# Optimization experiments

Measured on AMD Instinct MI355X. Metric: run time of the kernel, lower is better.

The kernel has to match this reference:

```python
import jax, jax.numpy as jnp
import numpy as np

DIM = 256
HEADS = 8
CAMS = 6
MINSIZE = 25  # AdaptiveAvgPool2d output size = min(feature_map_size)


def layernorm(x, g, b, eps=1e-5):
    mu = x.mean(-1, keepdims=True)
    var = ((x - mu) ** 2).mean(-1, keepdims=True)
    return (x - mu) / jnp.sqrt(var + eps) * g + b


def setup_inputs() -> dict:
    key = jax.random.key(0)
    ks = jax.random.split(key, 16)
    d, n = DIM, CAMS
    s = 0.02
    inp = {}
    inp["q"] = jax.random.normal(ks[0], (2, n, d, 50, 50), jnp.float32)
    inp["k"] = jax.random.normal(ks[1], (2, n, d, 50, 50), jnp.float32)
    inp["v"] = jax.random.normal(ks[2], (2, n, d, 50, 50), jnp.float32)
    inp["Wq"] = jax.random.normal(ks[3], (d, d), jnp.float32) * s
    inp["bq"] = jnp.zeros((d,), jnp.float32)
    inp["Wk"] = jax.random.normal(ks[4], (d, d), jnp.float32) * s
    inp["bk"] = jnp.zeros((d,), jnp.float32)
    inp["Wv"] = jax.random.normal(ks[5], (d, d), jnp.float32) * s
    inp["bv"] = jnp.zeros((d,), jnp.float32)
    inp["Wproj"] = jax.random.normal(ks[6], (n * d, d), jnp.float32) * s
    inp["bproj"] = jnp.zeros((d,), jnp.float32)
    inp["Waddq"] = jax.random.normal(ks[7], (n * d, d), jnp.float32) * s
    inp["baddq"] = jnp.zeros((d,), jnp.float32)
    inp["W1"] = jax.random.normal(ks[8], (d, 2 * d), jnp.float32) * s
    inp["b1"] = jnp.zeros((2 * d,), jnp.float32)
    inp["W2"] = jax.random.normal(ks[9], (2 * d, d), jnp.float32) * s
    inp["b2"] = jnp.zeros((d,), jnp.float32)
    inp["g_pre"] = jnp.ones((n * d,), jnp.float32)
    inp["b_pre"] = jnp.zeros((n * d,), jnp.float32)
    inp["g_norm"] = jnp.ones((d,), jnp.float32)
    inp["b_norm"] = jnp.zeros((d,), jnp.float32)
    return inp


def reference(q, k, v, Wq, bq, Wk, bk, Wv, bv, Wproj, bproj, Waddq, baddq,
              W1, b1, W2, b2, g_pre, b_pre, g_norm, b_norm):
    B, n, d, H, W = q.shape
    m = HEADS
    dh = d // m
    Q = H * W

    # residual query path: (b n d H W) -> (b HW (n d)) -> add_qproj -> (b HW d)
    add_q = jnp.transpose(q, (0, 3, 4, 1, 2)).reshape(B, Q, n * d) @ Waddq + baddq

    # queries: (b n d H W) -> (b n HW d) -> to_q
    qf = jnp.transpose(q, (0, 1, 3, 4, 2)).reshape(B, n, Q, d) @ Wq + bq

    # adaptive avg pool to MINSIZE (exact 2x2 bins since 50 = 2*25)
    def pool(t):
        _, _, _, h, w = t.shape
        return t.reshape(B, n, d, MINSIZE, h // MINSIZE, MINSIZE, w // MINSIZE).mean((4, 6))

    kp = pool(k)  # (b n d 25 25)
    vp = pool(v)
    K = MINSIZE * MINSIZE
    # (avg pool commutes with the pointwise linear to_k/to_v)
    kf = jnp.transpose(kp, (0, 1, 3, 4, 2)).reshape(B, n, K, d) @ Wk + bk
    vf = jnp.transpose(vp, (0, 1, 3, 4, 2)).reshape(B, n, K, d) @ Wv + bv

    # split heads
    qh = qf.reshape(B, n, Q, m, dh)
    kh = kf.reshape(B, n, K, m, dh)
    vh = vf.reshape(B, n, K, m, dh)

    # per-camera scores, softmax jointly over concatenated camera keys
    scores = (dh ** -0.5) * jnp.einsum('bnqmd,bnkmd->bmqnk', qh, kh)  # (B,m,Q,n,K)
    attn = jax.nn.softmax(scores.reshape(B, m, Q, n * K), axis=-1).reshape(B, m, Q, n, K)

    # per-camera attention output, concat cams (and heads within each cam) -> (B,Q,n*d)
    out = jnp.einsum('bmqnk,bnkmd->bqnmd', attn, vh).reshape(B, Q, n * d)

    x = layernorm(out, g_pre, b_pre) @ Wproj + bproj  # (B,Q,d)
    x = x + add_q
    h1 = jax.nn.gelu(x @ W1 + b1, approximate=False)
    x = x + layernorm(h1 @ W2 + b2, g_norm, b_norm)
    return jnp.transpose(x.reshape(B, H, W, d), (0, 3, 1, 2))  # (B,d,H,W)
```

## Files before the change

### kernel.cpp

```cpp
#include <hip/hip_runtime.h>
#include <math.h>

#define BATCH 2
#define NCAM 6
#define DIM 256
#define HEADS 8
#define DH 32
#define HW 2500
#define KP 625
#define NDIM (NCAM*DIM)

#define SCALE_LOG2E 0.25503488494404f

typedef __attribute__((ext_vector_type(8))) short short8;
typedef __attribute__((ext_vector_type(4))) float f32x4;

__device__ __forceinline__ short f2bf(float f) {
    union { float f; unsigned u; } v; v.f = f;
    unsigned r = v.u + 0x7fffu + ((v.u >> 16) & 1u);
    return (short)(r >> 16);
}
__device__ __forceinline__ float bf2f(short h) {
    union { unsigned u; float f; } v; v.u = ((unsigned)(unsigned short)h) << 16;
    return v.f;
}
__device__ __forceinline__ float exp2_hw(float x) {
    return __builtin_amdgcn_exp2f(x);
}

struct WJ { const float* src; short* dst; int K, N; };
struct WArgs { WJ j[7]; };

__global__ __launch_bounds__(256) void prep_all(
    const float* __restrict__ q, const float* __restrict__ k,
    const float* __restrict__ v, short* __restrict__ qbf,
    short* __restrict__ kpbf, short* __restrict__ vpbf, WArgs wa)
{
    __shared__ float t[32][33];
    const int tx = threadIdx.x & 31, ty = threadIdx.x >> 5;
    int i = blockIdx.x;
    if (i < 7584) {
        int slab = i / 632, rem = i % 632;
        int hwB = (rem % 79) * 32, dB = (rem / 79) * 32;
        const float* src = q + (size_t)slab * 640000;
#pragma unroll
        for (int ii = 0; ii < 32; ii += 8) {
            int hw = hwB + tx;
            t[ty + ii][tx] = (hw < HW) ? src[(size_t)(dB + ty + ii) * HW + hw] : 0.f;
        }
        __syncthreads();
#pragma unroll
        for (int ii = 0; ii < 32; ii += 8) {
            int hw = hwB + ty + ii;
            if (hw < HW)
                qbf[((size_t)slab * HW + hw) * DIM + dB + tx] = f2bf(t[tx][ty + ii]);
        }
    } else if (i < 11424) {
        int i2 = i - 7584;
        const float* base; short* dst;
        if (i2 < 1920) { base = k; dst = kpbf; }
        else           { base = v; dst = vpbf; i2 -= 1920; }
        int slab = i2 / 160, rem = i2 % 160;
        int kpB = (rem % 20) * 32, dB = (rem / 20) * 32;
        const float* src = base + (size_t)slab * 640000;
        dst += (size_t)slab * (KP * DIM);
#pragma unroll
        for (int ii = 0; ii < 32; ii += 8) {
            int kp = kpB + tx;
            float val = 0.f;
            if (kp < KP) {
                int r2 = (kp / 25) * 2, c2 = (kp % 25) * 2;
                const float* p0 = src + (size_t)(dB + ty + ii) * HW + r2 * 50 + c2;
                val = 0.25f * (p0[0] + p0[1] + p0[50] + p0[51]);
            }
            t[ty + ii][tx] = val;
        }
        __syncthreads();
#pragma unroll
        for (int ii = 0; ii < 32; ii += 8) {
            int kp = kpB + ty + ii;
            if (kp < KP)
                dst[(size_t)kp * DIM + dB + tx] = f2bf(t[tx][ty + ii]);
        }
    } else {
        int wi = i - 11424;
        WJ jb = wa.j[0];
        for (int jj = 0; jj < 7; jj++) {
            jb = wa.j[jj];
            int cnt = (jb.K >> 5) * (jb.N >> 5);
            if (wi < cnt) break;
            wi -= cnt;
        }
        int tn = jb.N >> 5;
        int nB = (wi % tn) * 32, kB = (wi / tn) * 32;
#pragma unroll
        for (int ii = 0; ii < 32; ii += 8)
            t[ty + ii][tx] = jb.src[(size_t)(kB + ty + ii) * jb.N + nB + tx];
        __syncthreads();
#pragma unroll
        for (int ii = 0; ii < 32; ii += 8)
            jb.dst[(size_t)(nB + ty + ii) * jb.K + kB + tx] = f2bf(t[tx][ty + ii]);
    }
}

struct GJob { const short* A; const short* Bt; const float* bias;
              short* Cb; float* Cf; int M, Ks, Kl, kOff, mode; float smul; };
struct GArgs { GJob j[5]; int base[6]; };

__global__ __launch_bounds__(256) void gemm_in(GArgs ga) {
    int bid;
    {
        const int nwg = ga.base[5];
        int orig = blockIdx.x;
        int q8 = nwg >> 3, r8 = nwg & 7;
        int xcd = orig & 7, idx = orig >> 3;
        bid = (xcd < r8 ? xcd * (q8 + 1) : r8 * (q8 + 1) + (xcd - r8) * q8) + idx;
    }
    int jj = 0;
    while (bid >= ga.base[jj + 1]) jj++;
    GJob jb = ga.j[jj];
    const int local = bid - ga.base[jj];

    __shared__ short As[128 * 32];
    __shared__ short Bs[64 * 32];

    const int tid  = threadIdx.x;
    const int nB   = (local & 3) * 64;
    const int rB   = (local >> 2) * 128;
    const int w    = tid >> 6;
    const int lane = tid & 63;
    const int l15  = lane & 15;
    const int quad = lane >> 4;
    const int M = jb.M, Ks = jb.Ks, Kl = jb.Kl, kOff = jb.kOff;

    f32x4 acc[2][4];
#pragma unroll
    for (int i = 0; i < 2; i++)
#pragma unroll
        for (int jt = 0; jt < 4; jt++) acc[i][jt] = (f32x4){0.f, 0.f, 0.f, 0.f};

    const int ra = tid >> 1, k0 = (tid & 1) * 16;
    const int rga = rB + ra;
    const int bb = rga / 2500, hwp = rga % 2500;
    const int nb_ = tid >> 2, gkb = tid & 3;

    short8 pa0 = {0,0,0,0,0,0,0,0}, pa1 = pa0, pb = pa0;
    if (rga < M) {
        if (jb.mode) {
            int kk = kOff + k0;
            int cam = kk >> 8, c = kk & 255;
            const short* p = &jb.A[(((size_t)(bb * 6 + cam)) * HW + hwp) * DIM + c];
            pa0 = *(const short8*)p; pa1 = *(const short8*)(p + 8);
        } else {
            const short* p = &jb.A[(size_t)rga * Ks + kOff + k0];
            pa0 = *(const short8*)p; pa1 = *(const short8*)(p + 8);
        }
    }
    pb = *(const short8*)&jb.Bt[(size_t)(nB + nb_) * Ks + kOff + gkb * 8];

    for (int kB = 0; kB < Kl; kB += 32) {
        __syncthreads();
        {
            int g0 = k0 >> 3;
            *(short8*)&As[ra * 32 + ((g0 ^ (ra & 3)) << 3)]       = pa0;
            *(short8*)&As[ra * 32 + (((g0 + 1) ^ (ra & 3)) << 3)] = pa1;
            *(short8*)&Bs[nb_ * 32 + ((gkb ^ (nb_ & 3)) << 3)]    = pb;
        }
        __syncthreads();
        int kN = kB + 32;
        if (kN < Kl) {
            if (rga < M) {
                if (jb.mode) {
                    int kk = kOff + kN + k0;
                    int cam = kk >> 8, c = kk & 255;
                    const short* p = &jb.A[(((size_t)(bb * 6 + cam)) * HW + hwp) * DIM + c];
                    pa0 = *(const short8*)p; pa1 = *(const short8*)(p + 8);
                } else {
                    const short* p = &jb.A[(size_t)rga * Ks + kOff + kN + k0];
                    pa0 = *(const short8*)p; pa1 = *(const short8*)(p + 8);
                }
            }
            pb = *(const short8*)&jb.Bt[(size_t)(nB + nb_) * Ks + kOff + kN + gkb * 8];
        }
        short8 af[2], bfr[4];
#pragma unroll
        for (int i = 0; i < 2; i++) {
            int m = w * 32 + i * 16 + l15;
            af[i] = *(const short8*)&As[m * 32 + ((quad ^ (m & 3)) << 3)];
        }
#pragma unroll
        for (int jt = 0; jt < 4; jt++) {
            int n = jt * 16 + l15;
            bfr[jt] = *(const short8*)&Bs[n * 32 + ((quad ^ (n & 3)) << 3)];
        }
#pragma unroll
        for (int i = 0; i < 2; i++)
#pragma unroll
            for (int jt = 0; jt < 4; jt++)
                acc[i][jt] = __builtin_amdgcn_mfma_f32_16x16x32_bf16(
                    af[i], bfr[jt], acc[i][jt], 0, 0, 0);
    }
#pragma unroll
    for (int i = 0; i < 2; i++) {
        int rbase = rB + w * 32 + i * 16 + quad * 4;
#pragma unroll
        for (int jt = 0; jt < 4; jt++) {
            int col = nB + jt * 16 + l15;
            float bcol = jb.bias ? jb.bias[col] : 0.f;
#pragma unroll
            for (int reg = 0; reg < 4; reg++) {
                int rr = rbase + reg;
                if (rr < M) {
                    float vv = (acc[i][jt][reg] + bcol) * jb.smul;
                    if (jb.Cb) jb.Cb[(size_t)rr * 256 + col] = f2bf(vv);
                    else       jb.Cf[(size_t)rr * 256 + col] = vv;
                }
            }
        }
    }
}

template<int EPI, int WF32, int WBF>
__global__ __launch_bounds__(256) void mgemm_bf(
    const short* __restrict__ A, const short* __restrict__ Bt,
    const float* __restrict__ bias, const float* __restrict__ res,
    const float* __restrict__ res2,
    float* __restrict__ C, short* __restrict__ C2, int M, int N, int K)
{
    __shared__ short As[128 * 32];
    __shared__ short Bs[64 * 32];

    const int tid  = threadIdx.x;
    const int nB   = blockIdx.x * 64;
    const int rB   = blockIdx.y * 128;
    const int w    = tid >> 6;
    const int lane = tid & 63;
    const int l15  = lane & 15;
    const int quad = lane >> 4;

    f32x4 acc[2][4];
#pragma unroll
    for (int i = 0; i < 2; i++)
#pragma unroll
        for (int jt = 0; jt < 4; jt++) acc[i][jt] = (f32x4){0.f, 0.f, 0.f, 0.f};

    const int ra = tid >> 1, k0 = (tid & 1) * 16;
    const int rga = rB + ra;
    const int nb_ = tid >> 2, gkb = tid & 3;

    short8 pa0 = {0,0,0,0,0,0,0,0}, pa1 = pa0, pb = pa0;
    if (rga < M) {
        const short* p = &A[(size_t)rga * K + k0];
        pa0 = *(const short8*)p; pa1 = *(const short8*)(p + 8);
    }
    pb = *(const short8*)&Bt[(size_t)(nB + nb_) * K + gkb * 8];

    for (int kB = 0; kB < K; kB += 32) {
        __syncthreads();
        {
            int g0 = k0 >> 3;
            *(short8*)&As[ra * 32 + ((g0 ^ (ra & 3)) << 3)]       = pa0;
            *(short8*)&As[ra * 32 + (((g0 + 1) ^ (ra & 3)) << 3)] = pa1;
            *(short8*)&Bs[nb_ * 32 + ((gkb ^ (nb_ & 3)) << 3)]    = pb;
        }
        __syncthreads();
        int kN = kB + 32;
        if (kN < K) {
            if (rga < M) {
                const short* p = &A[(size_t)rga * K + kN + k0];
                pa0 = *(const short8*)p; pa1 = *(const short8*)(p + 8);
            }
            pb = *(const short8*)&Bt[(size_t)(nB + nb_) * K + kN + gkb * 8];
        }
        short8 af[2], bfr[4];
#pragma unroll
        for (int i = 0; i < 2; i++) {
            int m = w * 32 + i * 16 + l15;
            af[i] = *(const short8*)&As[m * 32 + ((quad ^ (m & 3)) << 3)];
        }
#pragma unroll
        for (int jt = 0; jt < 4; jt++) {
            int n = jt * 16 + l15;
            bfr[jt] = *(const short8*)&Bs[n * 32 + ((quad ^ (n & 3)) << 3)];
        }
#pragma unroll
        for (int i = 0; i < 2; i++)
#pragma unroll
            for (int jt = 0; jt < 4; jt++)
                acc[i][jt] = __builtin_amdgcn_mfma_f32_16x16x32_bf16(
                    af[i], bfr[jt], acc[i][jt], 0, 0, 0);
    }
#pragma unroll
    for (int i = 0; i < 2; i++) {
        int rbase = rB + w * 32 + i * 16 + quad * 4;
#pragma unroll
        for (int jt = 0; jt < 4; jt++) {
            int col = nB + jt * 16 + l15;
            float bcol = bias[col];
#pragma unroll
            for (int reg = 0; reg < 4; reg++) {
                int rr = rbase + reg;
                if (rr < M) {
                    float vv = acc[i][jt][reg] + bcol;
                    if (EPI == 1) vv = 0.5f * vv * (1.f + erff(vv * 0.70710678118654752f));
                    if (EPI == 2) {
                        vv += res[(size_t)rr * N + col];
                        if (res2) vv += res2[(size_t)rr * N + col];
                    }
                    if (WF32) C[(size_t)rr * N + col] = vv;
                    if (WBF)  C2[(size_t)rr * N + col] = f2bf(vv);
                }
            }
        }
    }
}

#define TQA 64
#define CH 64
#define VSTR 72

__global__ __launch_bounds__(256) void attn_mfma(
    const short* __restrict__ qf, const short* __restrict__ kf,
    const short* __restrict__ vf, short* __restrict__ attn_out,
    float* __restrict__ Zp)
{
    const int qt  = blockIdx.x;
    const int bm  = blockIdx.y;
    const int cam = blockIdx.z;
    const int b = bm >> 3, m = bm & 7;
    const int q0 = qt * TQA;
    const int tid = threadIdx.x;
    const int w = tid >> 6, lane = tid & 63;
    const int l15 = lane & 15, quad = lane >> 4;

    __shared__ __align__(16) short Ks[CH][DH];
    __shared__ __align__(16) short Vt[DH][VSTR];

    const size_t slab = (size_t)(b * 6 + cam);

    int qrow = q0 + w * 16 + l15;
    int qcl  = qrow < HW ? qrow : HW - 1;
    const short8 aq = *(const short8*)&qf[(slab * HW + qcl) * DIM + m * DH + quad * 8];

    const short* kb = kf + slab * KP * DIM + m * DH;
    const short* vb = vf + slab * KP * DIM + m * DH;

    f32x4 oacc[2];
    oacc[0] = (f32x4){0.f, 0.f, 0.f, 0.f};
    oacc[1] = (f32x4){0.f, 0.f, 0.f, 0.f};
    float zp = 0.f;

    const int kl = tid >> 2, d8 = (tid & 3) * 8;
    const int jtw  = ((kl >> 5) & 1) | (((kl >> 2) & 1) << 1);
    const int rw   = (((kl >> 3) & 3) << 2) | (kl & 3);
    const int krow = jtw * 16 + rw;
    const int kp2 = tid >> 3, dv = (tid & 7) * 4;
    const int vcol2 = (((kp2 >> 2) ^ (dv >> 3)) << 3) | ((2 * kp2) & 7);

    for (int c0 = 0; c0 < KP; c0 += CH) {
        __syncthreads();
        {
            int key = c0 + kl;
            short8 kv8 = {0, 0, 0, 0, 0, 0, 0, 0};
            if (key < KP) kv8 = *(const short8*)&kb[(size_t)key * DIM + d8];
            *(short8*)&Ks[krow][d8] = kv8;

            int k0v = c0 + 2 * kp2;
            uint2 a0 = {0u, 0u}, a1 = {0u, 0u};
            if (k0v < KP)     a0 = *(const uint2*)&vb[(size_t)k0v * DIM + dv];
            if (k0v + 1 < KP) a1 = *(const uint2*)&vb[(size_t)(k0v + 1) * DIM + dv];
            *(unsigned*)&Vt[dv + 0][vcol2] = __builtin_amdgcn_perm(a1.x, a0.x, 0x05040100u);
            *(unsigned*)&Vt[dv + 1][vcol2] = __builtin_amdgcn_perm(a1.x, a0.x, 0x07060302u);
            *(unsigned*)&Vt[dv + 2][vcol2] = __builtin_amdgcn_perm(a1.y, a0.y, 0x05040100u);
            *(unsigned*)&Vt[dv + 3][vcol2] = __builtin_amdgcn_perm(a1.y, a0.y, 0x07060302u);
        }
        __syncthreads();
        f32x4 sfragT[4];
#pragma unroll
        for (int jt = 0; jt < 4; jt++) {
            short8 bk8 = *(const short8*)&Ks[jt * 16 + l15][quad * 8];
            sfragT[jt] = __builtin_amdgcn_mfma_f32_16x16x32_bf16(
                bk8, aq, (f32x4){0.f, 0.f, 0.f, 0.f}, 0, 0, 0);
        }
        union PA { unsigned u[4]; short8 s8; } pa[2];
        if (c0 + CH <= KP) {
#pragma unroll
            for (int jt = 0; jt < 4; jt++) {
                float e0 = exp2_hw(sfragT[jt][0]);
                float e1 = exp2_hw(sfragT[jt][1]);
                float e2 = exp2_hw(sfragT[jt][2]);
                float e3 = exp2_hw(sfragT[jt][3]);
                zp += (e0 + e1) + (e2 + e3);
                asm("v_cvt_pk_bf16_f32 %0, %1, %2"
                    : "=v"(pa[jt & 1].u[(jt >> 1) * 2]) : "v"(e0), "v"(e1));
                asm("v_cvt_pk_bf16_f32 %0, %1, %2"
                    : "=v"(pa[jt & 1].u[(jt >> 1) * 2 + 1]) : "v"(e2), "v"(e3));
            }
        } else {
            int kq8 = c0 + quad * 8;
#pragma unroll
            for (int jt = 0; jt < 4; jt++) {
                int kb0 = kq8 + (jt & 1) * 32 + ((jt >> 1) << 2);
                float e0 = (kb0 + 0 < KP) ? exp2_hw(sfragT[jt][0]) : 0.f;
                float e1 = (kb0 + 1 < KP) ? exp2_hw(sfragT[jt][1]) : 0.f;
                float e2 = (kb0 + 2 < KP) ? exp2_hw(sfragT[jt][2]) : 0.f;
                float e3 = (kb0 + 3 < KP) ? exp2_hw(sfragT[jt][3]) : 0.f;
                zp += (e0 + e1) + (e2 + e3);
                asm("v_cvt_pk_bf16_f32 %0, %1, %2"
                    : "=v"(pa[jt & 1].u[(jt >> 1) * 2]) : "v"(e0), "v"(e1));
                asm("v_cvt_pk_bf16_f32 %0, %1, %2"
                    : "=v"(pa[jt & 1].u[(jt >> 1) * 2 + 1]) : "v"(e2), "v"(e3));
            }
        }
#pragma unroll
        for (int ks = 0; ks < 2; ks++) {
#pragma unroll
            for (int nt = 0; nt < 2; nt++) {
                int dhn = nt * 16 + l15;
                int pgrp = ((ks * 4 + quad) ^ (dhn >> 3));
                short8 bv8 = *(const short8*)&Vt[dhn][pgrp << 3];
                oacc[nt] = __builtin_amdgcn_mfma_f32_16x16x32_bf16(
                    pa[ks].s8, bv8, oacc[nt], 0, 0, 0);
            }
        }
    }
    zp += __shfl_xor(zp, 16, 64);
    zp += __shfl_xor(zp, 32, 64);
    if (quad == 0) {
        int q = q0 + w * 16 + l15;
        if (q < HW) Zp[((size_t)bm * 6 + cam) * HW + q] = zp;
    }
#pragma unroll
    for (int reg = 0; reg < 4; reg++) {
        int q = q0 + w * 16 + quad * 4 + reg;
        if (q < HW) {
            size_t rowb = ((size_t)b * HW + q) * NDIM + cam * DIM + m * DH;
            attn_out[rowb + l15]      = f2bf(oacc[0][reg]);
            attn_out[rowb + 16 + l15] = f2bf(oacc[1][reg]);
        }
    }
}

__global__ __launch_bounds__(256) void ln_pre_kernel(
    const short* __restrict__ xin, short* __restrict__ lnbf,
    const float* __restrict__ Zp,
    const float* __restrict__ g, const float* __restrict__ bt)
{
    const int row = blockIdx.x;
    const int tid = threadIdx.x;
    const int b = row / 2500, q = row % 2500;
    __shared__ float zinv[8];
    if (tid < 8) {
        float z = 0.f;
#pragma unroll
        for (int cam = 0; cam < 6; cam++)
            z += Zp[((size_t)(b * 8 + tid) * 6 + cam) * HW + q];
        zinv[tid] = 1.f / z;
    }
    __syncthreads();
    const short* p = xin + (size_t)row * NDIM;
    float v[6];
    float s = 0.f, ss = 0.f;
#pragma unroll
    for (int i = 0; i < 6; i++) {
        int c = tid + i * 256;
        v[i] = bf2f(p[c]) * zinv[(c >> 5) & 7];
        s += v[i]; ss += v[i] * v[i];
    }
    __shared__ float rs[4], rss[4];
    int lane = tid & 63, wid = tid >> 6;
#pragma unroll
    for (int o = 32; o > 0; o >>= 1) { s += __shfl_down(s, o); ss += __shfl_down(ss, o); }
    if (lane == 0) { rs[wid] = s; rss[wid] = ss; }
    __syncthreads();
    s = rs[0] + rs[1] + rs[2] + rs[3];
    ss = rss[0] + rss[1] + rss[2] + rss[3];
    float mu = s * (1.f / NDIM);
    float var = ss * (1.f / NDIM) - mu * mu;
    float inv = rsqrtf(var + 1e-5f);
#pragma unroll
    for (int i = 0; i < 6; i++) {
        int c = tid + i * 256;
        lnbf[(size_t)row * NDIM + c] = f2bf((v[i] - mu) * inv * g[c] + bt[c]);
    }
}

__global__ __launch_bounds__(256) void final_kernel2(
    const float* __restrict__ x, const float* __restrict__ y2,
    const float* __restrict__ g, const float* __restrict__ bt,
    float* __restrict__ out)
{
    __shared__ float T[256][33];
    __shared__ float ps[32][8], pss[32][8];
    __shared__ float mu_s[32], inv_s[32];
    const int tid = threadIdx.x;
    const int rl = tid & 31, seg = tid >> 5;
    const int r0 = blockIdx.x * 32;
    const int row = r0 + rl;
    const bool ok = row < 5000;

    float4 yv[8];
    float s = 0.f, ss = 0.f;
    if (ok) {
        const float4* yp = (const float4*)(y2 + (size_t)row * DIM + seg * 32);
#pragma unroll
        for (int j = 0; j < 8; j++) {
            yv[j] = yp[j];
            s += yv[j].x + yv[j].y + yv[j].z + yv[j].w;
            ss += yv[j].x * yv[j].x + yv[j].y * yv[j].y
                + yv[j].z * yv[j].z + yv[j].w * yv[j].w;
        }
    } else {
#pragma unroll
        for (int j = 0; j < 8; j++) yv[j] = (float4){0, 0, 0, 0};
    }
    ps[rl][seg] = s; pss[rl][seg] = ss;
    __syncthreads();
    if (tid < 32) {
        float a = 0.f, b2 = 0.f;
#pragma unroll
        for (int j = 0; j < 8; j++) { a += ps[tid][j]; b2 += pss[tid][j]; }
        float mu = a * (1.f / DIM);
        float var = b2 * (1.f / DIM) - mu * mu;
        mu_s[tid] = mu;
        inv_s[tid] = rsqrtf(var + 1e-5f);
    }
    __syncthreads();
    if (ok) {
        float mu = mu_s[rl], inv = inv_s[rl];
        const float4* xp = (const float4*)(x + (size_t)row * DIM + seg * 32);
#pragma unroll
        for (int j = 0; j < 8; j++) {
            float4 xv = xp[j];
            int c = seg * 32 + j * 4;
            T[c + 0][rl] = xv.x + (yv[j].x - mu) * inv * g[c + 0] + bt[c + 0];
            T[c + 1][rl] = xv.y + (yv[j].y - mu) * inv * g[c + 1] + bt[c + 1];
            T[c + 2][rl] = xv.z + (yv[j].z - mu) * inv * g[c + 2] + bt[c + 2];
            T[c + 3][rl] = xv.w + (yv[j].w - mu) * inv * g[c + 3] + bt[c + 3];
        }
    }
    __syncthreads();
    const int w = tid >> 6, lane = tid & 63;
    const int hl = lane & 31, ch = lane >> 5;
    const int rr = r0 + hl;
    if (rr < 5000) {
        int b = rr / 2500, hw = rr % 2500;
        size_t obase = (size_t)b * 640000 + hw;
#pragma unroll
        for (int it = 0; it < 32; it++) {
            int c = it * 8 + w * 2 + ch;
            out[obase + (size_t)c * 2500] = T[c][hl];
        }
    }
}

extern "C" void kernel_launch(void* const* d_in, const int* in_sizes, int n_in,
                              void* d_out, int out_size, void* d_ws, size_t ws_size,
                              hipStream_t stream)
{
    const float* q     = (const float*)d_in[0];
    const float* k     = (const float*)d_in[1];
    const float* v     = (const float*)d_in[2];
    const float* Wq    = (const float*)d_in[3];
    const float* bq    = (const float*)d_in[4];
    const float* Wk    = (const float*)d_in[5];
    const float* bk    = (const float*)d_in[6];
    const float* Wv    = (const float*)d_in[7];
    const float* bv    = (const float*)d_in[8];
    const float* Wproj = (const float*)d_in[9];
    const float* bproj = (const float*)d_in[10];
    const float* Waddq = (const float*)d_in[11];
    const float* baddq = (const float*)d_in[12];
    const float* W1    = (const float*)d_in[13];
    const float* b1    = (const float*)d_in[14];
    const float* W2    = (const float*)d_in[15];
    const float* b2    = (const float*)d_in[16];
    const float* g_pre = (const float*)d_in[17];
    const float* b_pre = (const float*)d_in[18];
    const float* g_nrm = (const float*)d_in[19];
    const float* b_nrm = (const float*)d_in[20];
    float* out = (float*)d_out;

    float* ws = (float*)d_ws;
    short* qf_a   = (short*)(ws);
    short* lnbf   = (short*)(ws);
    short* qbf    = (short*)(ws + 3840000);
    short* kf_a   = (short*)(ws + 7680000);
    short* kpbf   = (short*)(ws + 8640000);
    short* vf_a   = (short*)(ws + 9600000);
    short* vpbf   = (short*)(ws + 10560000);
    float* add_q  = ws + 11520000;
    short* attn_o = (short*)(ws + 12800000);
    short* xbf    = (short*)(ws + 12800000);
    short* h1bf   = (short*)(ws + 13440000);
    float* add_q2 = ws + 16640000;
    float* x      = ws + 20480000;
    float* Zp     = ws + 21760000;
    short* eW     = (short*)(ws + 22000000);
    short* Wq_t    = eW;
    short* Wk_t    = eW + 65536;
    short* Wv_t    = eW + 131072;
    short* Waddq_t = eW + 196608;
    short* lW     = (short*)(ws + 22295000);
    short* Wproj_t = lW;
    short* W1_t    = lW + 393216;
    short* W2_t    = lW + 524288;
    float* y2     = ws + 22625000;

    dim3 blk(256);

    {
        WArgs wa;
        wa.j[0] = {Wq,    Wq_t,    256,  256};
        wa.j[1] = {Wk,    Wk_t,    256,  256};
        wa.j[2] = {Wv,    Wv_t,    256,  256};
        wa.j[3] = {Waddq, Waddq_t, 1536, 256};
        wa.j[4] = {Wproj, Wproj_t, 1536, 256};
        wa.j[5] = {W1,    W1_t,    256,  512};
        wa.j[6] = {W2,    W2_t,    512,  256};
        prep_all<<<dim3(12640), blk, 0, stream>>>(q, k, v, qbf, kpbf, vpbf, wa);
    }
    {
        GArgs ga;
        ga.j[0] = {qbf,  Waddq_t, baddq,   nullptr, add_q,  5000,  1536, 768, 0,   1, 1.0f};
        ga.j[1] = {qbf,  Waddq_t, nullptr, nullptr, add_q2, 5000,  1536, 768, 768, 1, 1.0f};
        ga.j[2] = {qbf,  Wq_t,    bq,      qf_a,    nullptr, 30000, 256, 256, 0,   0, SCALE_LOG2E};
        ga.j[3] = {kpbf, Wk_t,    bk,      kf_a,    nullptr, 7500,  256, 256, 0,   0, 1.0f};
        ga.j[4] = {vpbf, Wv_t,    bv,      vf_a,    nullptr, 7500,  256, 256, 0,   0, 1.0f};
        int cnt[5] = {160, 160, 940, 236, 236};
        ga.base[0] = 0;
        for (int i = 0; i < 5; i++) ga.base[i + 1] = ga.base[i] + cnt[i];
        gemm_in<<<dim3(ga.base[5]), blk, 0, stream>>>(ga);
    }
    attn_mfma<<<dim3(40, 16, 6), blk, 0, stream>>>(qf_a, kf_a, vf_a, attn_o, Zp);
    ln_pre_kernel<<<dim3(5000), blk, 0, stream>>>(attn_o, lnbf, Zp, g_pre, b_pre);
    mgemm_bf<2, 1, 1><<<dim3(4, 40), blk, 0, stream>>>(
        lnbf, Wproj_t, bproj, add_q, add_q2, x, xbf, 5000, 256, 1536);
    mgemm_bf<1, 0, 1><<<dim3(8, 40), blk, 0, stream>>>(
        xbf, W1_t, b1, nullptr, nullptr, nullptr, h1bf, 5000, 512, 256);
    mgemm_bf<0, 1, 0><<<dim3(4, 40), blk, 0, stream>>>(
        h1bf, W2_t, b2, nullptr, nullptr, y2, nullptr, 5000, 256, 512);
    final_kernel2<<<dim3(157), blk, 0, stream>>>(x, y2, g_nrm, b_nrm, out);
}
```

Measured before the change: 334.1 us.

## Double-buffer LDS tiles in input GEMM and drop XCD block remapping

Converts the input-projection GEMM main loop to double-buffered shared memory. The next tile is staged while the current one is consumed, and global loads run two tiles ahead, so only one barrier is needed per K-step instead of two. It also removes the XCD-aware block index remapping and uses blockIdx.x directly, which may change L2 locality across chiplets. Shared memory use doubles, which could reduce occupancy.

Measured after the change: 317.7 us. 4.9% less time.

```diff
diff --git a/kernel.cpp b/kernel.cpp
--- a/kernel.cpp
+++ b/kernel.cpp
@@ -108,21 +108,14 @@
 struct GArgs { GJob j[5]; int base[6]; };
 
 __global__ __launch_bounds__(256) void gemm_in(GArgs ga) {
-    int bid;
-    {
-        const int nwg = ga.base[5];
-        int orig = blockIdx.x;
-        int q8 = nwg >> 3, r8 = nwg & 7;
-        int xcd = orig & 7, idx = orig >> 3;
-        bid = (xcd < r8 ? xcd * (q8 + 1) : r8 * (q8 + 1) + (xcd - r8) * q8) + idx;
-    }
+    int bid = blockIdx.x;
     int jj = 0;
     while (bid >= ga.base[jj + 1]) jj++;
     GJob jb = ga.j[jj];
     const int local = bid - ga.base[jj];
 
-    __shared__ short As[128 * 32];
-    __shared__ short Bs[64 * 32];
+    __shared__ short As[2][128 * 32];
+    __shared__ short Bs[2][64 * 32];
 
     const int tid  = threadIdx.x;
     const int nB   = (local & 3) * 64;
@@ -131,7 +124,8 @@
     const int lane = tid & 63;
     const int l15  = lane & 15;
     const int quad = lane >> 4;
-    const int M = jb.M, Ks = jb.Ks, Kl = jb.Kl, kOff = jb.kOff;
+    const int M = jb.M, Ks = jb.Ks, kOff = jb.kOff;
+    const int nT = jb.Kl >> 5;
 
     f32x4 acc[2][4];
 #pragma unroll
@@ -143,55 +137,51 @@
     const int rga = rB + ra;
     const int bb = rga / 2500, hwp = rga % 2500;
     const int nb_ = tid >> 2, gkb = tid & 3;
+    const int g0 = k0 >> 3;
 
     short8 pa0 = {0,0,0,0,0,0,0,0}, pa1 = pa0, pb = pa0;
-    if (rga < M) {
-        if (jb.mode) {
-            int kk = kOff + k0;
-            int cam = kk >> 8, c = kk & 255;
-            const short* p = &jb.A[(((size_t)(bb * 6 + cam)) * HW + hwp) * DIM + c];
-            pa0 = *(const short8*)p; pa1 = *(const short8*)(p + 8);
-        } else {
-            const short* p = &jb.A[(size_t)rga * Ks + kOff + k0];
-            pa0 = *(const short8*)p; pa1 = *(const short8*)(p + 8);
-        }
-    }
-    pb = *(const short8*)&jb.Bt[(size_t)(nB + nb_) * Ks + kOff + gkb * 8];
-
-    for (int kB = 0; kB < Kl; kB += 32) {
-        __syncthreads();
-        {
-            int g0 = k0 >> 3;
-            *(short8*)&As[ra * 32 + ((g0 ^ (ra & 3)) << 3)]       = pa0;
-            *(short8*)&As[ra * 32 + (((g0 + 1) ^ (ra & 3)) << 3)] = pa1;
-            *(short8*)&Bs[nb_ * 32 + ((gkb ^ (nb_ & 3)) << 3)]    = pb;
-        }
-        __syncthreads();
-        int kN = kB + 32;
-        if (kN < Kl) {
-            if (rga < M) {
-                if (jb.mode) {
-                    int kk = kOff + kN + k0;
-                    int cam = kk >> 8, c = kk & 255;
-                    const short* p = &jb.A[(((size_t)(bb * 6 + cam)) * HW + hwp) * DIM + c];
-                    pa0 = *(const short8*)p; pa1 = *(const short8*)(p + 8);
-                } else {
-                    const short* p = &jb.A[(size_t)rga * Ks + kOff + kN + k0];
-                    pa0 = *(const short8*)p; pa1 = *(const short8*)(p + 8);
-                }
-            }
-            pb = *(const short8*)&jb.Bt[(size_t)(nB + nb_) * Ks + kOff + kN + gkb * 8];
-        }
+
+#define GLOADT(t) do {                                                        \
+        int kk = kOff + (t) * 32 + k0;                                        \
+        if (rga < M) {                                                        \
+            const short* p;                                                   \
+            if (jb.mode) {                                                    \
+                int cam = kk >> 8, c = kk & 255;                              \
+                p = &jb.A[(((size_t)(bb * 6 + cam)) * HW + hwp) * DIM + c];   \
+            } else {                                                          \
+                p = &jb.A[(size_t)rga * Ks + kk];                             \
+            }                                                                 \
+            pa0 = *(const short8*)p; pa1 = *(const short8*)(p + 8);           \
+        }                                                                     \
+        pb = *(const short8*)&jb.Bt[(size_t)(nB + nb_) * Ks                   \
+                                    + kOff + (t) * 32 + gkb * 8];             \
+    } while (0)
+
+#define STAGET(bf) do {                                                       \
+        *(short8*)&As[bf][ra * 32 + ((g0 ^ (ra & 3)) << 3)]       = pa0;      \
+        *(short8*)&As[bf][ra * 32 + (((g0 + 1) ^ (ra & 3)) << 3)] = pa1;      \
+        *(short8*)&Bs[bf][nb_ * 32 + ((gkb ^ (nb_ & 3)) << 3)]    = pb;       \
+    } while (0)
+
+    GLOADT(0);
+    STAGET(0);
+    if (nT > 1) GLOADT(1);
+    __syncthreads();
+
+    int cur = 0;
+    for (int t = 0; t < nT; t++) {
+        if (t + 1 < nT) STAGET(cur ^ 1);
+        if (t + 2 < nT) GLOADT(t + 2);
         short8 af[2], bfr[4];
 #pragma unroll
         for (int i = 0; i < 2; i++) {
             int m = w * 32 + i * 16 + l15;
-            af[i] = *(const short8*)&As[m * 32 + ((quad ^ (m & 3)) << 3)];
+            af[i] = *(const short8*)&As[cur][m * 32 + ((quad ^ (m & 3)) << 3)];
         }
 #pragma unroll
         for (int jt = 0; jt < 4; jt++) {
             int n = jt * 16 + l15;
-            bfr[jt] = *(const short8*)&Bs[n * 32 + ((quad ^ (n & 3)) << 3)];
+            bfr[jt] = *(const short8*)&Bs[cur][n * 32 + ((quad ^ (n & 3)) << 3)];
         }
 #pragma unroll
         for (int i = 0; i < 2; i++)
@@ -199,7 +189,11 @@
             for (int jt = 0; jt < 4; jt++)
                 acc[i][jt] = __builtin_amdgcn_mfma_f32_16x16x32_bf16(
                     af[i], bfr[jt], acc[i][jt], 0, 0, 0);
-    }
+        if (t + 1 < nT) { __syncthreads(); cur ^= 1; }
+    }
+#undef GLOADT
+#undef STAGET
+
 #pragma unroll
     for (int i = 0; i < 2; i++) {
         int rbase = rB + w * 32 + i * 16 + quad * 4;
```
